# Kernel tuning notes

Measured on AMD Instinct MI355X. Metric: run time of the kernel, lower is better.

Reference implementation:

```python
import jax, jax.numpy as jnp
import numpy as np

B, N, D, OUT, NUM_ITERS = 8, 4096, 1024, 1024, 3
LN_EPS = 1e-5


def setup_inputs() -> dict:
    key = jax.random.key(0)
    ks = jax.random.split(key, 8)
    s = (6.0 / (2 * D)) ** 0.5  # xavier-uniform-like scale
    return {
        "query": jax.random.normal(ks[0], (B, D), jnp.float32),
        "feat": jax.random.normal(ks[1], (B, N, D), jnp.float32),
        "W_h": jax.random.uniform(ks[2], (D, D), jnp.float32, -s, s),
        "W_f": jax.random.uniform(ks[3], (D, D), jnp.float32, -s, s),
        "W_g": jax.random.normal(ks[4], (4, D, D), jnp.float32) / np.sqrt(D),
        "ln_w": jnp.ones((D,), jnp.float32),
        "ln_b": jnp.zeros((D,), jnp.float32),
        "W_out": jax.random.uniform(ks[5], (OUT, D), jnp.float32, -s, s),
        "b_out": jnp.zeros((OUT,), jnp.float32),
        "feat_mask": jax.random.bernoulli(ks[6], 0.2, (B, 1, 1, N)),
    }


def _layer_norm(x, w, b):
    mu = x.mean(-1, keepdims=True)
    var = jnp.var(x, axis=-1, keepdims=True)
    return (x - mu) / jnp.sqrt(var + LN_EPS) * w + b


def reference(query, feat, W_h, W_f, W_g, ln_w, ln_b, W_out, b_out, feat_mask):
    q = query @ W_h                       # [B, D]
    f = feat @ W_f                        # [B, N, D]
    mask = feat_mask.reshape(feat.shape[0], feat.shape[1])  # squeeze(1).squeeze(1)
    b = jnp.where(mask, jnp.float32(-1e18), jnp.float32(0.0))  # [B, N]
    # feat_group is iteration-invariant: mean over the 4 orthogonal transforms
    # mean_g(f @ W_g[g].T) == f @ mean_g(W_g).T
    fg = f @ W_g.mean(0).T                # [B, N, D]
    n = fg.shape[1]
    for i in range(NUM_ITERS):
        c = jax.nn.softmax(b, axis=1)     # [B, N]
        if i == NUM_ITERS - 1:
            out = jnp.einsum('bn,bnd->bd', c, fg)
        else:
            delta = jnp.einsum('bd,bnd->bn', q, fg)
            delta = (delta - delta.mean(1, keepdims=True)) / (
                delta.std(1, keepdims=True, ddof=1) + 1e-9)  # torch.std is unbiased
            b = b + delta
            out = jnp.einsum('bn,bnd->bd', c, fg) / n  # mean over dim 1
        q = _layer_norm(q + jax.nn.selu(out), ln_w, ln_b)
    return q @ W_out.T + b_out
```

## Files before the change

### kernel.cpp

```cpp
#include <hip/hip_runtime.h>
#include <hip/hip_bf16.h>


using u16 = unsigned short;
using u32 = unsigned int;
using u8  = unsigned char;
using u64 = unsigned long long;

#define SELU_L 1.0507009873554805f
#define SELU_A 1.6732632423543772f

__device__ float g_M[1048576];
__device__ float g_q[8192];
__device__ float g_tus[24576];
__device__ float g_bst[32768];
__device__ float g_c[32768];
__device__ float g_delta[32768];
__device__ float g_outv[8192];
__device__ float g_v[8192];
__device__ int   g_dt[12];

__device__ __forceinline__ float blo(u32 u){ return __uint_as_float(u << 16); }
__device__ __forceinline__ float bhi(u32 u){ return __uint_as_float(u & 0xffff0000u); }
__device__ __forceinline__ float b2f(u16 u){ return __uint_as_float(((u32)u) << 16); }

__device__ __forceinline__ void unpack8(uint4 x, float* f){
  f[0]=blo(x.x); f[1]=bhi(x.x); f[2]=blo(x.y); f[3]=bhi(x.y);
  f[4]=blo(x.z); f[5]=bhi(x.z); f[6]=blo(x.w); f[7]=bhi(x.w);
}

__device__ __forceinline__ float ldf(const void* p, size_t i, int dt){
  return dt ? ((const float*)p)[i] : b2f(((const u16*)p)[i]);
}
__device__ __forceinline__ void load8(const void* base, size_t idx, int dt, float* f){
  if (dt == 0) {
    uint4 x = *(const uint4*)((const u16*)base + idx);
    unpack8(x, f);
  } else {
    const float* p = (const float*)base + idx;
    float4 a = *(const float4*)p, b = *(const float4*)(p + 4);
    f[0]=a.x; f[1]=a.y; f[2]=a.z; f[3]=a.w; f[4]=b.x; f[5]=b.y; f[6]=b.z; f[7]=b.w;
  }
}

__device__ __forceinline__ float wredsum(float x){
#pragma unroll
  for (int o = 32; o; o >>= 1) x += __shfl_xor(x, o, 64);
  return x;
}

__global__ void kdet(const void* p0, const void* p1, const void* p2, const void* p3,
                     const void* p4, const void* p5, const void* p6, const void* p7,
                     const void* p8, const void* p9)
{
  const void* ps[10] = {p0,p1,p2,p3,p4,p5,p6,p7,p8,p9};
  int tid = threadIdx.x;
  int w = tid >> 6, lane = tid & 63;
  if (w < 9) {
    const u16* wp = (const u16*)ps[w];
    u16 x0 = wp[lane], x1 = wp[64 + lane];
    int e0 = (x0 >> 7) & 0xFF, e1 = (x1 >> 7) & 0xFF;
    u64 nz0 = __ballot(x0 != 0), nz1 = __ballot(x1 != 0);
    u64 pa0 = __ballot(x0 != 0 && e0 >= 0x70 && e0 <= 0x8F);
    u64 pa1 = __ballot(x1 != 0 && e1 >= 0x70 && e1 <= 0x8F);
    if (lane == 0) {
      const u64 evenm = 0x5555555555555555ULL;
      int nz = __popcll(nz0) + __popcll(nz1);
      int pass = __popcll(pa0) + __popcll(pa1);
      int evenNZ = __popcll(nz0 & evenm) + __popcll(nz1 & evenm);
      int oddNZ  = nz - evenNZ;
      int dt;
      if (nz == 0)                    dt = 0;
      else if (evenNZ == 0 && oddNZ)  dt = 1;
      else                            dt = (pass * 10 >= nz * 9) ? 0 : 1;
      g_dt[w] = dt;
    }
  } else if (w == 9) {
    const u8* mp = (const u8*)ps[9];
    u64 v = ((const u64*)mp)[lane];
    bool f16c=false, isF=false, nz01=false, nzNon4=false, nzM8_4=false, anynz=false;
#pragma unroll
    for (int j = 0; j < 8; ++j) {
      u8 cb = (u8)(v >> (8 * j));
      if (!cb) continue;
      int i = lane * 8 + j;
      anynz = true;
      if (cb == 0x3C && (i & 1)) f16c = true;
      if (cb == 0x3F || cb == 0x80) isF = true;
      int m = i & 3;
      if (m == 0 || m == 1) nz01 = true;
      if (m != 0) nzNon4 = true;
      if ((i & 7) == 4) nzM8_4 = true;
    }
    bool A  = __ballot(f16c)   != 0;
    bool Bf = __ballot(isF)    != 0;
    bool C  = __ballot(nz01)   != 0;
    bool Dn = __ballot(nzNon4) != 0;
    bool E  = __ballot(nzM8_4) != 0;
    bool F  = __ballot(anynz)  != 0;
    if (lane == 0) {
      int mode;
      if (A)       mode = 4;
      else if (Bf) mode = C ? 2 : 3;
      else if (Dn) mode = 0;
      else if (E)  mode = 1;
      else if (F)  mode = 5;
      else         mode = 1;
      g_dt[9] = mode;
    }
  }
  for (int i = tid; i < 8192; i += 640) g_q[i] = 0.f;
}

__global__ void kzero() {
  int i = (blockIdx.x * 256 + threadIdx.x) * 4;
  *(float4*)(g_tus + i) = make_float4(0.f, 0.f, 0.f, 0.f);
}

__global__ void kprep(const void* __restrict__ Wg, const void* __restrict__ Wh,
                      const void* __restrict__ query, const u8* __restrict__ maskp)
{
  int blk = blockIdx.x, tid = threadIdx.x;
  if (blk < 1024) {
    int dtg = g_dt[4];
    int e = blk * 1024 + tid * 4;
    float a0=0.f,a1=0.f,a2=0.f,a3=0.f;
#pragma unroll
    for (int g = 0; g < 4; ++g) {
      size_t o = (size_t)g * 1048576 + e;
      a0 += ldf(Wg, o+0, dtg); a1 += ldf(Wg, o+1, dtg);
      a2 += ldf(Wg, o+2, dtg); a3 += ldf(Wg, o+3, dtg);
    }
    *(float4*)(g_M + e) = make_float4(a0*0.25f, a1*0.25f, a2*0.25f, a3*0.25f);
  } else if (blk < 1088) {
    int dtq = g_dt[0], dth = g_dt[2];
    __shared__ float ql[512];
    int blk2 = blk - 1024;
    int kt = blk2 & 3, dc = blk2 >> 2;
    for (int idx = tid; idx < 512; idx += 256) {
      int b = idx >> 6, d = idx & 63;
      ql[idx] = ldf(query, b * 1024 + dc * 64 + d, dtq);
    }
    __syncthreads();
    int k = kt * 256 + tid;
    float acc[8] = {0,0,0,0,0,0,0,0};
    for (int dd = 0; dd < 64; ++dd) {
      int d = dc * 64 + dd;
      float w = ldf(Wh, (size_t)d * 1024 + k, dth);
#pragma unroll
      for (int b = 0; b < 8; ++b) acc[b] += ql[(b << 6) + dd] * w;
    }
#pragma unroll
    for (int b = 0; b < 8; ++b) atomicAdd(&g_q[b * 1024 + k], acc[b]);
  } else {
    int mode = g_dt[9];
    int e0 = (blk - 1088) * 1024 + tid * 4;
#pragma unroll
    for (int j = 0; j < 4; ++j) {
      int e = e0 + j;
      bool on;
      if (mode == 0)      on = maskp[e] != 0;
      else if (mode == 1) on = ((const int*)maskp)[e] != 0;
      else if (mode == 2) on = ((const u16*)maskp)[e] != 0;
      else if (mode == 3) on = ((const u32*)maskp)[e] != 0;
      else if (mode == 4) on = ((const u16*)maskp)[e] != 0;
      else                on = ((const u64*)maskp)[e] != 0ULL;
      g_bst[e] = on ? -1e18f : 0.f;
    }
  }
}

__global__ void ksm(int do_t)
{
  __shared__ float sm[1024];
  int blk = blockIdx.x, tid = threadIdx.x;
  float* t = g_tus;
  if (blk < 8) {
    int b = blk;
    const float* row = g_bst + b * 4096;
    float mx = -3.4e38f;
    for (int i = tid; i < 4096; i += 256) mx = fmaxf(mx, row[i]);
    sm[tid] = mx; __syncthreads();
    for (int s2 = 128; s2; s2 >>= 1) { if (tid < s2) sm[tid] = fmaxf(sm[tid], sm[tid + s2]); __syncthreads(); }
    mx = sm[0]; __syncthreads();
    float sum = 0.f;
    for (int i = tid; i < 4096; i += 256) {
      float e = __expf(row[i] - mx);
      g_c[b * 4096 + i] = e; sum += e;
    }
    sm[tid] = sum; __syncthreads();
    for (int s2 = 128; s2; s2 >>= 1) { if (tid < s2) sm[tid] += sm[tid + s2]; __syncthreads(); }
    float inv = 1.f / sm[0];
    for (int i = tid; i < 4096; i += 256) g_c[b * 4096 + i] *= inv;
  } else {
    int blk2 = blk - 8;
    int jt = blk2 & 3, dc = blk2 >> 2;
    for (int idx = tid; idx < 512; idx += 256) {
      int b = idx >> 6, d = idx & 63;
      sm[idx] = g_q[b * 1024 + dc * 64 + d];
    }
    __syncthreads();
    int j = jt * 256 + tid;
    float acc[8] = {0,0,0,0,0,0,0,0};
    for (int dd = 0; dd < 64; ++dd) {
      int d = dc * 64 + dd;
      float mv = g_M[(size_t)d * 1024 + j];
#pragma unroll
      for (int b = 0; b < 8; ++b) acc[b] += sm[(b << 6) + dd] * mv;
    }
#pragma unroll
    for (int b = 0; b < 8; ++b) atomicAdd(&t[b * 1024 + j], acc[b]);
  }
}

__global__ void kv(const void* __restrict__ Wf)
{
  __shared__ float tl[8192];
  int tid = threadIdx.x;
  int dtf = g_dt[3];
  for (int i = tid; i < 8192; i += 256) tl[i] = g_tus[i];
  __syncthreads();
  int w = tid >> 6, lane = tid & 63;
  int k = blockIdx.x * 4 + w;
  size_t row = (size_t)k * 1024;
  float f[16];
  load8(Wf, row + lane * 8, dtf, f);
  load8(Wf, row + 512 + lane * 8, dtf, f + 8);
  float acc[8];
#pragma unroll
  for (int b = 0; b < 8; ++b) {
    const float* tb = tl + b * 1024;
    float d = 0.f;
#pragma unroll
    for (int j = 0; j < 8; ++j) d += f[j]     * tb[lane * 8 + j];
#pragma unroll
    for (int j = 0; j < 8; ++j) d += f[8 + j] * tb[512 + lane * 8 + j];
    acc[b] = wredsum(d);
  }
  if (lane == 0) {
#pragma unroll
    for (int b = 0; b < 8; ++b) g_v[b * 1024 + k] = acc[b];
  }
}

__global__ void __launch_bounds__(256)
kfeat(const void* __restrict__ feat, int need_delta)
{
  __shared__ float sl[4][1024];
  int tid = threadIdx.x, w = tid >> 6, lane = tid & 63;
  int b = blockIdx.x >> 6, ch = blockIdx.x & 63;
  int dtf = g_dt[1];
  float* s = g_tus + 16384;
  float vr[16];
#pragma unroll
  for (int j = 0; j < 16; ++j) vr[j] = 0.f;
  if (need_delta) {
    const float* vb = g_v + b * 1024;
#pragma unroll
    for (int j = 0; j < 8; ++j) { vr[j] = vb[lane * 8 + j]; vr[8 + j] = vb[512 + lane * 8 + j]; }
  }
  float acc[16];
#pragma unroll
  for (int j = 0; j < 16; ++j) acc[j] = 0.f;
  int n0 = ch * 64 + w * 16;
  for (int r = 0; r < 16; ++r) {
    int n = n0 + r;
    size_t row = ((size_t)b * 4096 + n) * 1024;
    float f[16];
    load8(feat, row + lane * 8, dtf, f);
    load8(feat, row + 512 + lane * 8, dtf, f + 8);
    float cn = g_c[b * 4096 + n];
#pragma unroll
    for (int j = 0; j < 16; ++j) acc[j] += cn * f[j];
    if (need_delta) {
      float dot = 0.f;
#pragma unroll
      for (int j = 0; j < 16; ++j) dot += f[j] * vr[j];
      dot = wredsum(dot);
      if (lane == 0) g_delta[b * 4096 + n] = dot;
    }
  }
#pragma unroll
  for (int j = 0; j < 8; ++j) {
    sl[w][lane * 8 + j] = acc[j];
    sl[w][512 + lane * 8 + j] = acc[8 + j];
  }
  __syncthreads();
#pragma unroll
  for (int j = 0; j < 4; ++j) {
    int k = tid * 4 + j;
    float val = sl[0][k] + sl[1][k] + sl[2][k] + sl[3][k];
    atomicAdd(&s[b * 1024 + k], val);
  }
}

__global__ void kpost(const void* __restrict__ Wf, int do_stats)
{
  __shared__ float sm[1024];
  int blk = blockIdx.x, tid = threadIdx.x;
  float* u = g_tus + 8192;
  float* s = g_tus + 16384;
  if (do_stats && blk < 8) {
    int b = blk;
    const float* row = g_delta + b * 4096;
    float xs[16], sum = 0.f, sq = 0.f;
#pragma unroll
    for (int r = 0; r < 16; ++r) { float x = row[tid + 256 * r]; xs[r] = x; sum += x; sq += x * x; }
    sm[tid] = sum; __syncthreads();
    for (int s2 = 128; s2; s2 >>= 1) { if (tid < s2) sm[tid] += sm[tid + s2]; __syncthreads(); }
    sum = sm[0]; __syncthreads();
    sm[tid] = sq; __syncthreads();
    for (int s2 = 128; s2; s2 >>= 1) { if (tid < s2) sm[tid] += sm[tid + s2]; __syncthreads(); }
    sq = sm[0];
    float mean = sum / 4096.f;
    float var = fmaxf((sq - 4096.f * mean * mean) / 4095.f, 0.f);
    float inv = 1.f / (sqrtf(var) + 1e-9f);
#pragma unroll
    for (int r = 0; r < 16; ++r) {
      int i = tid + 256 * r;
      g_bst[b * 4096 + i] += (xs[r] - mean) * inv;
    }
  } else {
    int dtf = g_dt[3];
    int blk2 = blk - (do_stats ? 8 : 0);
    int jt = blk2 & 3, kc = blk2 >> 2;
    for (int idx = tid; idx < 512; idx += 256) {
      int b = idx >> 6, kk = idx & 63;
      sm[idx] = s[b * 1024 + kc * 64 + kk];
    }
    __syncthreads();
    int j = jt * 256 + tid;
    float acc[8] = {0,0,0,0,0,0,0,0};
    for (int kk = 0; kk < 64; ++kk) {
      int k = kc * 64 + kk;
      float w = ldf(Wf, (size_t)k * 1024 + j, dtf);
#pragma unroll
      for (int b = 0; b < 8; ++b) acc[b] += sm[(b << 6) + kk] * w;
    }
#pragma unroll
    for (int b = 0; b < 8; ++b) atomicAdd(&u[b * 1024 + j], acc[b]);
  }
}

__global__ void kout()
{
  __shared__ float ul[8192];
  int tid = threadIdx.x;
  for (int i = tid; i < 8192; i += 256) ul[i] = g_tus[8192 + i];
  __syncthreads();
  int w = tid >> 6, lane = tid & 63;
  int d = blockIdx.x * 4 + w;
  const float* row = g_M + (size_t)d * 1024;
  float f[16];
#pragma unroll
  for (int cc = 0; cc < 4; ++cc) {
    float4 x = *(const float4*)(row + cc * 256 + lane * 4);
    f[cc*4+0]=x.x; f[cc*4+1]=x.y; f[cc*4+2]=x.z; f[cc*4+3]=x.w;
  }
  float acc[8];
#pragma unroll
  for (int b = 0; b < 8; ++b) {
    const float* ub = ul + b * 1024;
    float dd = 0.f;
#pragma unroll
    for (int cc = 0; cc < 4; ++cc)
#pragma unroll
      for (int e = 0; e < 4; ++e) dd += f[cc * 4 + e] * ub[cc * 256 + lane * 4 + e];
    acc[b] = wredsum(dd);
  }
  if (lane == 0) {
#pragma unroll
    for (int b = 0; b < 8; ++b) g_outv[b * 1024 + d] = acc[b];
  }
}

__global__ void kq(const void* __restrict__ lnw, const void* __restrict__ lnb,
                   float scale)
{
  __shared__ float sm[256];
  int b = blockIdx.x, tid = threadIdx.x;
  int dtw = g_dt[5], dtb = g_dt[6];
  float x[4], sum = 0.f, sq = 0.f;
#pragma unroll
  for (int j = 0; j < 4; ++j) {
    int d = tid * 4 + j;
    float o = g_outv[b * 1024 + d] * scale;
    float se = (o > 0.f) ? SELU_L * o : SELU_L * SELU_A * expm1f(o);
    float val = g_q[b * 1024 + d] + se;
    x[j] = val; sum += val; sq += val * val;
  }
  sm[tid] = sum; __syncthreads();
  for (int s2 = 128; s2; s2 >>= 1) { if (tid < s2) sm[tid] += sm[tid + s2]; __syncthreads(); }
  sum = sm[0]; __syncthreads();
  sm[tid] = sq; __syncthreads();
  for (int s2 = 128; s2; s2 >>= 1) { if (tid < s2) sm[tid] += sm[tid + s2]; __syncthreads(); }
  sq = sm[0];
  float mean = sum / 1024.f;
  float var = fmaxf(sq / 1024.f - mean * mean, 0.f);
  float rstd = rsqrtf(var + 1e-5f);
#pragma unroll
  for (int j = 0; j < 4; ++j) {
    int d = tid * 4 + j;
    g_q[b * 1024 + d] = (x[j] - mean) * rstd * ldf(lnw, d, dtw) + ldf(lnb, d, dtb);
  }
}

__global__ void kfin(const void* __restrict__ Wout, const void* __restrict__ bout,
                     float* __restrict__ out)
{
  __shared__ float ql[8192];
  int tid = threadIdx.x;
  int dto = g_dt[7], dtb = g_dt[8];
  for (int i = tid; i < 8192; i += 256) ql[i] = g_q[i];
  __syncthreads();
  int w = tid >> 6, lane = tid & 63;
  int o = blockIdx.x * 4 + w;
  size_t row = (size_t)o * 1024;
  float f[16];
  load8(Wout, row + lane * 8, dto, f);
  load8(Wout, row + 512 + lane * 8, dto, f + 8);
  float acc[8];
#pragma unroll
  for (int b = 0; b < 8; ++b) {
    const float* qb = ql + b * 1024;
    float d = 0.f;
#pragma unroll
    for (int j = 0; j < 8; ++j) d += f[j]     * qb[lane * 8 + j];
#pragma unroll
    for (int j = 0; j < 8; ++j) d += f[8 + j] * qb[512 + lane * 8 + j];
    acc[b] = wredsum(d);
  }
  if (lane == 0) {
    float bo = ldf(bout, o, dtb);
#pragma unroll
    for (int b = 0; b < 8; ++b) out[b * 1024 + o] = acc[b] + bo;
  }
}

extern "C" void kernel_launch(void* const* d_in, const int* in_sizes, int n_in,
                              void* d_out, int out_size, void* d_ws, size_t ws_size,
                              hipStream_t stream)
{
  const void* query = d_in[0];
  const void* feat  = d_in[1];
  const void* Wh    = d_in[2];
  const void* Wf    = d_in[3];
  const void* Wg    = d_in[4];
  const void* lnw   = d_in[5];
  const void* lnb   = d_in[6];
  const void* Wout  = d_in[7];
  const void* bout  = d_in[8];
  const u8*   maskp = (const u8*)d_in[9];
  (void)in_sizes; (void)n_in; (void)out_size; (void)d_ws; (void)ws_size;

  kdet<<<1, 640, 0, stream>>>(query, feat, Wh, Wf, Wg, lnw, lnb, Wout, bout, maskp);
  kprep<<<1120, 256, 0, stream>>>(Wg, Wh, query, maskp);

  for (int i = 0; i < 3; ++i) {
    int nl = (i < 2);
    kzero<<<24, 256, 0, stream>>>();
    ksm<<<8 + (nl ? 64 : 0), 256, 0, stream>>>(nl);
    if (nl) kv<<<256, 256, 0, stream>>>(Wf);
    kfeat<<<512, 256, 0, stream>>>(feat, nl);
    kpost<<<(nl ? 8 : 0) + 64, 256, 0, stream>>>(Wf, nl);
    kout<<<256, 256, 0, stream>>>();
    kq<<<8, 256, 0, stream>>>(lnw, lnb, nl ? (1.f / 4096.f) : 1.f);
  }
  kfin<<<256, 256, 0, stream>>>(Wout, bout, (float*)d_out);
}
```

Baseline: 430.2 us.

## Fuse zeroing, softmax and layernorm into neighbouring kernels and widen matvec grids

Removes the separate kzero, ksm and kq launches. Buffer zeroing and the softmax now run as extra blocks in kt, kfd and kout, and the LayerNorm/SELU update is recomputed redundantly per block inside kt and kfin. The first softmax is computed directly from the mask count in kprep. The M and Wf matvecs are split into 16-row chunks over 256 blocks instead of 64-row chunks over 64 blocks, which adds parallelism at the cost of more atomics. The aim is fewer launches and less serial small-kernel latency, in exchange for duplicated LayerNorm work in every block.

```diff
diff --git a/kernel.cpp b/kernel.cpp
--- a/kernel.cpp
+++ b/kernel.cpp
@@ -12,11 +12,15 @@
 
 __device__ float g_M[1048576];
 __device__ float g_q[8192];
-__device__ float g_tus[24576];
+__device__ float g_qc[8192];
+__device__ float g_t[8192];
+__device__ float g_u[8192];
+__device__ float g_s[8192];
 __device__ float g_bst[32768];
 __device__ float g_c[32768];
 __device__ float g_delta[32768];
 __device__ float g_outv[8192];
+__device__ float g_outv2[8192];
 __device__ float g_v[8192];
 __device__ int   g_dt[12];
 
@@ -47,6 +51,14 @@
 #pragma unroll
   for (int o = 32; o; o >>= 1) x += __shfl_xor(x, o, 64);
   return x;
+}
+
+__device__ __forceinline__ bool mon(const u8* maskp, int e, int mode){
+  if (mode == 0) return maskp[e] != 0;
+  if (mode == 1) return ((const int*)maskp)[e] != 0;
+  if (mode == 2 || mode == 4) return ((const u16*)maskp)[e] != 0;
+  if (mode == 3) return ((const u32*)maskp)[e] != 0;
+  return ((const u64*)maskp)[e] != 0ULL;
 }
 
 __global__ void kdet(const void* p0, const void* p1, const void* p2, const void* p3,
@@ -109,16 +121,14 @@
       g_dt[9] = mode;
     }
   }
-  for (int i = tid; i < 8192; i += 640) g_q[i] = 0.f;
-}
-
-__global__ void kzero() {
-  int i = (blockIdx.x * 256 + threadIdx.x) * 4;
-  *(float4*)(g_tus + i) = make_float4(0.f, 0.f, 0.f, 0.f);
-}
-
-__global__ void kprep(const void* __restrict__ Wg, const void* __restrict__ Wh,
-                      const void* __restrict__ query, const u8* __restrict__ maskp)
+  for (int i = tid; i < 8192; i += 640) {
+    g_q[i] = 0.f; g_t[i] = 0.f; g_u[i] = 0.f; g_s[i] = 0.f;
+  }
+}
+
+__global__ void __launch_bounds__(256)
+kprep(const void* __restrict__ Wg, const void* __restrict__ Wh,
+      const void* __restrict__ query, const u8* __restrict__ maskp)
 {
   int blk = blockIdx.x, tid = threadIdx.x;
   if (blk < 1024) {
@@ -152,73 +162,118 @@
     }
 #pragma unroll
     for (int b = 0; b < 8; ++b) atomicAdd(&g_q[b * 1024 + k], acc[b]);
-  } else {
+  } else if (blk < 1120) {
     int mode = g_dt[9];
     int e0 = (blk - 1088) * 1024 + tid * 4;
 #pragma unroll
     for (int j = 0; j < 4; ++j) {
       int e = e0 + j;
-      bool on;
-      if (mode == 0)      on = maskp[e] != 0;
-      else if (mode == 1) on = ((const int*)maskp)[e] != 0;
-      else if (mode == 2) on = ((const u16*)maskp)[e] != 0;
-      else if (mode == 3) on = ((const u32*)maskp)[e] != 0;
-      else if (mode == 4) on = ((const u16*)maskp)[e] != 0;
-      else                on = ((const u64*)maskp)[e] != 0ULL;
-      g_bst[e] = on ? -1e18f : 0.f;
-    }
-  }
-}
-
-__global__ void ksm(int do_t)
-{
-  __shared__ float sm[1024];
+      g_bst[e] = mon(maskp, e, mode) ? -1e18f : 0.f;
+    }
+  } else {
+    __shared__ int sc[256];
+    int mode = g_dt[9];
+    int b = blk - 1120;
+    u32 bits = 0; int cnt = 0;
+#pragma unroll
+    for (int r = 0; r < 16; ++r) {
+      int n = tid + 256 * r;
+      bool on = mon(maskp, b * 4096 + n, mode);
+      if (on) bits |= (1u << r); else ++cnt;
+    }
+    sc[tid] = cnt; __syncthreads();
+    for (int s2 = 128; s2; s2 >>= 1) { if (tid < s2) sc[tid] += sc[tid + s2]; __syncthreads(); }
+    int ct = sc[0];
+    float inv = 1.f / (float)(ct ? ct : 4096);
+    float moff = ct ? 0.f : inv;
+#pragma unroll
+    for (int r = 0; r < 16; ++r) {
+      int n = tid + 256 * r;
+      g_c[b * 4096 + n] = ((bits >> r) & 1u) ? moff : inv;
+    }
+  }
+}
+
+__device__ __forceinline__ void build_ql(float* ql, const float* qsrc,
+                                         const float* osrc, float scale,
+                                         const void* lnw, const void* lnb, int tid)
+{
+  int w = tid >> 6, lane = tid & 63;
+  int dtw = g_dt[5], dtb = g_dt[6];
+#pragma unroll
+  for (int rr = 0; rr < 2; ++rr) {
+    int b = w + rr * 4;
+    const float* qb = qsrc + b * 1024;
+    const float* ob = osrc + b * 1024;
+    float x[16]; float sum = 0.f, sq = 0.f;
+#pragma unroll
+    for (int cc = 0; cc < 4; ++cc) {
+      float4 qv = *(const float4*)(qb + cc * 256 + lane * 4);
+      float4 ov = *(const float4*)(ob + cc * 256 + lane * 4);
+      float q4[4] = {qv.x, qv.y, qv.z, qv.w};
+      float o4[4] = {ov.x, ov.y, ov.z, ov.w};
+#pragma unroll
+      for (int e = 0; e < 4; ++e) {
+        float o = o4[e] * scale;
+        float se = (o > 0.f) ? SELU_L * o : SELU_L * SELU_A * expm1f(o);
+        float val = q4[e] + se;
+        x[cc * 4 + e] = val; sum += val; sq += val * val;
+      }
+    }
+    sum = wredsum(sum); sq = wredsum(sq);
+    float mean = sum * (1.f / 1024.f);
+    float var = fmaxf(sq * (1.f / 1024.f) - mean * mean, 0.f);
+    float rstd = rsqrtf(var + 1e-5f);
+#pragma unroll
+    for (int cc = 0; cc < 4; ++cc)
+#pragma unroll
+      for (int e = 0; e < 4; ++e) {
+        int d = cc * 256 + lane * 4 + e;
+        ql[b * 1024 + d] = (x[cc * 4 + e] - mean) * rstd * ldf(lnw, d, dtw)
+                           + ldf(lnb, d, dtb);
+      }
+  }
+  __syncthreads();
+}
+
+__global__ void __launch_bounds__(256)
+kt(const void* __restrict__ lnw, const void* __restrict__ lnb, int phase)
+{
+  __shared__ float ql[8192];
   int blk = blockIdx.x, tid = threadIdx.x;
-  float* t = g_tus;
-  if (blk < 8) {
-    int b = blk;
-    const float* row = g_bst + b * 4096;
-    float mx = -3.4e38f;
-    for (int i = tid; i < 4096; i += 256) mx = fmaxf(mx, row[i]);
-    sm[tid] = mx; __syncthreads();
-    for (int s2 = 128; s2; s2 >>= 1) { if (tid < s2) sm[tid] = fmaxf(sm[tid], sm[tid + s2]); __syncthreads(); }
-    mx = sm[0]; __syncthreads();
-    float sum = 0.f;
-    for (int i = tid; i < 4096; i += 256) {
-      float e = __expf(row[i] - mx);
-      g_c[b * 4096 + i] = e; sum += e;
-    }
-    sm[tid] = sum; __syncthreads();
-    for (int s2 = 128; s2; s2 >>= 1) { if (tid < s2) sm[tid] += sm[tid + s2]; __syncthreads(); }
-    float inv = 1.f / sm[0];
-    for (int i = tid; i < 4096; i += 256) g_c[b * 4096 + i] *= inv;
+  if (blk >= 256) {
+    int b = blk - 256;
+    *(float4*)(g_u + b * 1024 + tid * 4) = make_float4(0.f, 0.f, 0.f, 0.f);
+    return;
+  }
+  if (phase == 0) {
+    for (int i = tid; i < 8192; i += 256) ql[i] = g_q[i];
+    __syncthreads();
   } else {
-    int blk2 = blk - 8;
-    int jt = blk2 & 3, dc = blk2 >> 2;
-    for (int idx = tid; idx < 512; idx += 256) {
-      int b = idx >> 6, d = idx & 63;
-      sm[idx] = g_q[b * 1024 + dc * 64 + d];
-    }
-    __syncthreads();
-    int j = jt * 256 + tid;
-    float acc[8] = {0,0,0,0,0,0,0,0};
-    for (int dd = 0; dd < 64; ++dd) {
-      int d = dc * 64 + dd;
-      float mv = g_M[(size_t)d * 1024 + j];
-#pragma unroll
-      for (int b = 0; b < 8; ++b) acc[b] += sm[(b << 6) + dd] * mv;
-    }
-#pragma unroll
-    for (int b = 0; b < 8; ++b) atomicAdd(&t[b * 1024 + j], acc[b]);
-  }
-}
-
-__global__ void kv(const void* __restrict__ Wf)
-{
-  __shared__ float tl[8192];
+    build_ql(ql, g_qc, g_outv, 1.f / 4096.f, lnw, lnb, tid);
+  }
+  if (blk == 0) {
+    for (int i = tid; i < 8192; i += 256) g_qc[i] = ql[i];
+  }
+  int jt = blk & 3, dc4 = blk >> 2;
+  int j = jt * 256 + tid;
+  float acc[8] = {0,0,0,0,0,0,0,0};
+  for (int dd = 0; dd < 16; ++dd) {
+    int d = dc4 * 16 + dd;
+    float mv = g_M[(size_t)d * 1024 + j];
+#pragma unroll
+    for (int b = 0; b < 8; ++b) acc[b] += ql[(b << 10) + d] * mv;
+  }
+#pragma unroll
+  for (int b = 0; b < 8; ++b) atomicAdd(&g_t[b * 1024 + j], acc[b]);
+}
+
+__global__ void __launch_bounds__(256) kv(const void* __restrict__ Wf)
+{
+  __shared__ float shm[8192];
   int tid = threadIdx.x;
   int dtf = g_dt[3];
-  for (int i = tid; i < 8192; i += 256) tl[i] = g_tus[i];
+  for (int i = tid; i < 8192; i += 256) shm[i] = g_t[i];
   __syncthreads();
   int w = tid >> 6, lane = tid & 63;
   int k = blockIdx.x * 4 + w;
@@ -229,7 +284,7 @@
   float acc[8];
 #pragma unroll
   for (int b = 0; b < 8; ++b) {
-    const float* tb = tl + b * 1024;
+    const float* tb = shm + b * 1024;
     float d = 0.f;
 #pragma unroll
     for (int j = 0; j < 8; ++j) d += f[j]     * tb[lane * 8 + j];
@@ -244,13 +299,18 @@
 }
 
 __global__ void __launch_bounds__(256)
-kfeat(const void* __restrict__ feat, int need_delta)
+kfd(const void* __restrict__ feat, int need_delta)
 {
   __shared__ float sl[4][1024];
-  int tid = threadIdx.x, w = tid >> 6, lane = tid & 63;
-  int b = blockIdx.x >> 6, ch = blockIdx.x & 63;
+  int blkx = blockIdx.x, tid = threadIdx.x;
+  if (blkx >= 512) {
+    int b = blkx - 512;
+    *(float4*)(g_u + b * 1024 + tid * 4) = make_float4(0.f, 0.f, 0.f, 0.f);
+    return;
+  }
+  int w = tid >> 6, lane = tid & 63;
+  int b = blkx >> 6, ch = blkx & 63;
   int dtf = g_dt[1];
-  float* s = g_tus + 16384;
   float vr[16];
 #pragma unroll
   for (int j = 0; j < 16; ++j) vr[j] = 0.f;
@@ -290,17 +350,17 @@
   for (int j = 0; j < 4; ++j) {
     int k = tid * 4 + j;
     float val = sl[0][k] + sl[1][k] + sl[2][k] + sl[3][k];
-    atomicAdd(&s[b * 1024 + k], val);
-  }
-}
-
-__global__ void kpost(const void* __restrict__ Wf, int do_stats)
-{
-  __shared__ float sm[1024];
+    atomicAdd(&g_s[b * 1024 + k], val);
+  }
+}
+
+__global__ void __launch_bounds__(256)
+ksu(const void* __restrict__ Wf, int do_stats)
+{
+  __shared__ float sm[256];
   int blk = blockIdx.x, tid = threadIdx.x;
-  float* u = g_tus + 8192;
-  float* s = g_tus + 16384;
-  if (do_stats && blk < 8) {
+  if (blk < 8) {
+    if (!do_stats) return;
     int b = blk;
     const float* row = g_delta + b * 4096;
     float xs[16], sum = 0.f, sq = 0.f;
@@ -320,36 +380,64 @@
       int i = tid + 256 * r;
       g_bst[b * 4096 + i] += (xs[r] - mean) * inv;
     }
-  } else {
-    int dtf = g_dt[3];
-    int blk2 = blk - (do_stats ? 8 : 0);
-    int jt = blk2 & 3, kc = blk2 >> 2;
-    for (int idx = tid; idx < 512; idx += 256) {
-      int b = idx >> 6, kk = idx & 63;
-      sm[idx] = s[b * 1024 + kc * 64 + kk];
-    }
-    __syncthreads();
-    int j = jt * 256 + tid;
-    float acc[8] = {0,0,0,0,0,0,0,0};
-    for (int kk = 0; kk < 64; ++kk) {
-      int k = kc * 64 + kk;
-      float w = ldf(Wf, (size_t)k * 1024 + j, dtf);
-#pragma unroll
-      for (int b = 0; b < 8; ++b) acc[b] += sm[(b << 6) + kk] * w;
-    }
-#pragma unroll
-    for (int b = 0; b < 8; ++b) atomicAdd(&u[b * 1024 + j], acc[b]);
-  }
-}
-
-__global__ void kout()
-{
-  __shared__ float ul[8192];
-  int tid = threadIdx.x;
-  for (int i = tid; i < 8192; i += 256) ul[i] = g_tus[8192 + i];
+    return;
+  }
+  int dtf = g_dt[3];
+  int blk2 = blk - 8;
+  int jt = blk2 & 3, kc4 = blk2 >> 2;
+  if (tid < 128) {
+    int b = tid >> 4, kk = tid & 15;
+    sm[tid] = g_s[b * 1024 + kc4 * 16 + kk];
+  }
+  __syncthreads();
+  int j = jt * 256 + tid;
+  float acc[8] = {0,0,0,0,0,0,0,0};
+  for (int kk = 0; kk < 16; ++kk) {
+    int k = kc4 * 16 + kk;
+    float w = ldf(Wf, (size_t)k * 1024 + j, dtf);
+#pragma unroll
+    for (int b = 0; b < 8; ++b) acc[b] += sm[(b << 4) + kk] * w;
+  }
+#pragma unroll
+  for (int b = 0; b < 8; ++b) atomicAdd(&g_u[b * 1024 + j], acc[b]);
+}
+
+__global__ void __launch_bounds__(256) kout(int dst2)
+{
+  __shared__ float sh[8192];
+  int blk = blockIdx.x, tid = threadIdx.x;
+  if (blk >= 256) {
+    if (blk < 264) {
+      int b = blk - 256;
+      const float* row = g_bst + b * 4096;
+      float mx = -3.4e38f;
+      for (int i = tid; i < 4096; i += 256) mx = fmaxf(mx, row[i]);
+      sh[tid] = mx; __syncthreads();
+      for (int s2 = 128; s2; s2 >>= 1) { if (tid < s2) sh[tid] = fmaxf(sh[tid], sh[tid + s2]); __syncthreads(); }
+      mx = sh[0]; __syncthreads();
+      float sum = 0.f;
+      for (int i = tid; i < 4096; i += 256) {
+        float e = __expf(row[i] - mx);
+        g_c[b * 4096 + i] = e; sum += e;
+      }
+      sh[tid] = sum; __syncthreads();
+      for (int s2 = 128; s2; s2 >>= 1) { if (tid < s2) sh[tid] += sh[tid + s2]; __syncthreads(); }
+      float inv = 1.f / sh[0];
+      for (int i = tid; i < 4096; i += 256) g_c[b * 4096 + i] *= inv;
+    } else if (blk < 272) {
+      int b = blk - 264;
+      *(float4*)(g_t + b * 1024 + tid * 4) = make_float4(0.f, 0.f, 0.f, 0.f);
+    } else {
+      int b = blk - 272;
+      *(float4*)(g_s + b * 1024 + tid * 4) = make_float4(0.f, 0.f, 0.f, 0.f);
+    }
+    return;
+  }
+  float* dst = dst2 ? g_outv2 : g_outv;
+  for (int i = tid; i < 8192; i += 256) sh[i] = g_u[i];
   __syncthreads();
   int w = tid >> 6, lane = tid & 63;
-  int d = blockIdx.x * 4 + w;
+  int d = blk * 4 + w;
   const float* row = g_M + (size_t)d * 1024;
   float f[16];
 #pragma unroll
@@ -360,7 +448,7 @@
   float acc[8];
 #pragma unroll
   for (int b = 0; b < 8; ++b) {
-    const float* ub = ul + b * 1024;
+    const float* ub = sh + b * 1024;
     float dd = 0.f;
 #pragma unroll
     for (int cc = 0; cc < 4; ++cc)
@@ -370,51 +458,22 @@
   }
   if (lane == 0) {
 #pragma unroll
-    for (int b = 0; b < 8; ++b) g_outv[b * 1024 + d] = acc[b];
-  }
-}
-
-__global__ void kq(const void* __restrict__ lnw, const void* __restrict__ lnb,
-                   float scale)
-{
-  __shared__ float sm[256];
-  int b = blockIdx.x, tid = threadIdx.x;
-  int dtw = g_dt[5], dtb = g_dt[6];
-  float x[4], sum = 0.f, sq = 0.f;
-#pragma unroll
-  for (int j = 0; j < 4; ++j) {
-    int d = tid * 4 + j;
-    float o = g_outv[b * 1024 + d] * scale;
-    float se = (o > 0.f) ? SELU_L * o : SELU_L * SELU_A * expm1f(o);
-    float val = g_q[b * 1024 + d] + se;
-    x[j] = val; sum += val; sq += val * val;
-  }
-  sm[tid] = sum; __syncthreads();
-  for (int s2 = 128; s2; s2 >>= 1) { if (tid < s2) sm[tid] += sm[tid + s2]; __syncthreads(); }
-  sum = sm[0]; __syncthreads();
-  sm[tid] = sq; __syncthreads();
-  for (int s2 = 128; s2; s2 >>= 1) { if (tid < s2) sm[tid] += sm[tid + s2]; __syncthreads(); }
-  sq = sm[0];
-  float mean = sum / 1024.f;
-  float var = fmaxf(sq / 1024.f - mean * mean, 0.f);
-  float rstd = rsqrtf(var + 1e-5f);
-#pragma unroll
-  for (int j = 0; j < 4; ++j) {
-    int d = tid * 4 + j;
-    g_q[b * 1024 + d] = (x[j] - mean) * rstd * ldf(lnw, d, dtw) + ldf(lnb, d, dtb);
-  }
-}
-
-__global__ void kfin(const void* __restrict__ Wout, const void* __restrict__ bout,
-                     float* __restrict__ out)
+    for (int b = 0; b < 8; ++b) dst[b * 1024 + d] = acc[b];
+  }
+}
+
+__global__ void __launch_bounds__(256)
+kfin(const void* __restrict__ Wout, const void* __restrict__ bout,
+     const void* __restrict__ lnw, const void* __restrict__ lnb,
+     float* __restrict__ out)
 {
   __shared__ float ql[8192];
   int tid = threadIdx.x;
-  int dto = g_dt[7], dtb = g_dt[8];
-  for (int i = tid; i < 8192; i += 256) ql[i] = g_q[i];
-  __syncthreads();
+  build_ql(ql, g_qc, g_outv, 1.f / 4096.f, lnw, lnb, tid);
+  build_ql(ql, ql, g_outv2, 1.f, lnw, lnb, tid);
   int w = tid >> 6, lane = tid & 63;
   int o = blockIdx.x * 4 + w;
+  int dto = g_dt[7], dtb = g_dt[8];
   size_t row = (size_t)o * 1024;
   float f[16];
   load8(Wout, row + lane * 8, dto, f);
@@ -454,17 +513,20 @@
   (void)in_sizes; (void)n_in; (void)out_size; (void)d_ws; (void)ws_size;
 
   kdet<<<1, 640, 0, stream>>>(query, feat, Wh, Wf, Wg, lnw, lnb, Wout, bout, maskp);
-  kprep<<<1120, 256, 0, stream>>>(Wg, Wh, query, maskp);
-
-  for (int i = 0; i < 3; ++i) {
-    int nl = (i < 2);
-    kzero<<<24, 256, 0, stream>>>();
-    ksm<<<8 + (nl ? 64 : 0), 256, 0, stream>>>(nl);
-    if (nl) kv<<<256, 256, 0, stream>>>(Wf);
-    kfeat<<<512, 256, 0, stream>>>(feat, nl);
-    kpost<<<(nl ? 8 : 0) + 64, 256, 0, stream>>>(Wf, nl);
-    kout<<<256, 256, 0, stream>>>();
-    kq<<<8, 256, 0, stream>>>(lnw, lnb, nl ? (1.f / 4096.f) : 1.f);
-  }
-  kfin<<<256, 256, 0, stream>>>(Wout, bout, (float*)d_out);
-}
+  kprep<<<1128, 256, 0, stream>>>(Wg, Wh, query, maskp);
+
+  kt<<<264, 256, 0, stream>>>(lnw, lnb, 0);
+  kv<<<256, 256, 0, stream>>>(Wf);
+  kfd<<<512, 256, 0, stream>>>(feat, 1);
+  ksu<<<264, 256, 0, stream>>>(Wf, 1);
+  kout<<<280, 256, 0, stream>>>(0);
+  kt<<<264, 256, 0, stream>>>(lnw, lnb, 1);
+  kv<<<256, 256, 0, stream>>>(Wf);
+  kfd<<<512, 256, 0, stream>>>(feat, 1);
+  ksu<<<264, 256, 0, stream>>>(Wf, 1);
+  kout<<<280, 256, 0, stream>>>(0);
+  kfd<<<520, 256, 0, stream>>>(feat, 0);
+  ksu<<<264, 256, 0, stream>>>(Wf, 0);
+  kout<<<256, 256, 0, stream>>>(1);
+  kfin<<<256, 256, 0, stream>>>(Wout, bout, lnw, lnb, (float*)d_out);
+}
```

New measurement: 421.8 us. Within noise of the previous version (-1.9%).
